# Kernel optimization log

Hardware: AMD Instinct MI355X
Metric: run time of the kernel (lower is better)

The kernel has to match this reference:

```python
import jax, jax.numpy as jnp
import numpy as np

NEG = -1e9  # large negative used as log(0) to keep grads finite
EPS = 1e-38


def _pcfg_inside(theta_log, Phi):
    # theta_log: [N,N,N] (A -> B C), Phi: [B,N,T] log terminal probs
    B, N, T = Phi.shape
    tm = jnp.max(theta_log)
    et = jnp.exp(theta_log - tm)  # [A,Bn,Cn], all > 0
    beta = jnp.full((B, N, T, T), NEG, dtype=Phi.dtype)
    idx = jnp.arange(T)
    beta = beta.at[:, :, idx, idx].set(Phi)  # length-1 spans
    for l in range(2, T + 1):
        P = T - l + 1
        ii = jnp.arange(P)
        ss = jnp.arange(l - 1)
        lcol = ii[:, None] + ss[None, :]          # left child end  [P,S]
        left = beta[:, :, ii[:, None], lcol]      # [B,N,P,S]
        right = beta[:, :, lcol + 1, (ii + l - 1)[:, None]]  # [B,N,P,S]
        ml = jnp.max(left, axis=1)                # [B,P,S]
        mr = jnp.max(right, axis=1)
        el = jnp.exp(left - ml[:, None])
        er = jnp.exp(right - mr[:, None])
        inner = jnp.einsum('xyz,byps,bzps->bxps', et, el, er)
        sc = jnp.log(jnp.maximum(inner, EPS)) + tm + ml[:, None] + mr[:, None]
        score = jax.scipy.special.logsumexp(sc, axis=-1)  # over split points -> [B,N,P]
        beta = beta.at[:, :, ii, ii + l - 1].set(score)
    logZ = beta[:, 0, 0, T - 1]  # start symbol id 0, full span
    return beta, logZ


def _pcfg_outside(theta_log, beta):
    B, N, T, _ = beta.shape
    tm = jnp.max(theta_log)
    et = jnp.exp(theta_log - tm)
    alpha = jnp.full((B, N, T, T), NEG, dtype=beta.dtype)
    alpha = alpha.at[:, 0, 0, T - 1].set(0.0)
    for l in range(T, 1, -1):  # parent spans, longest first
        P = T - l + 1
        ii = jnp.arange(P)
        jj = ii + l - 1
        ss = jnp.arange(l - 1)
        lcol = ii[:, None] + ss[None, :]          # left child end  [P,S]
        rrow = lcol + 1                            # right child start
        a = alpha[:, :, ii, jj]                    # [B,N,P]
        lb = beta[:, :, ii[:, None], lcol]         # [B,N,P,S]
        rb = beta[:, :, rrow, jj[:, None]]         # [B,N,P,S]
        ma = jnp.max(a, axis=1)                    # [B,P]
        ea = jnp.exp(a - ma[:, None])
        mrb = jnp.max(rb, axis=1)
        erb = jnp.exp(rb - mrb[:, None])
        mlb = jnp.max(lb, axis=1)
        elb = jnp.exp(lb - mlb[:, None])
        cL = jnp.log(jnp.maximum(jnp.einsum('xyz,bxp,bzps->byps', et, ea, erb), EPS)) \
             + tm + ma[:, None, :, None] + mrb[:, None]
        cR = jnp.log(jnp.maximum(jnp.einsum('xyz,bxp,byps->bzps', et, ea, elb), EPS)) \
             + tm + ma[:, None, :, None] + mlb[:, None]
        alpha = alpha.at[:, :, ii[:, None], lcol].set(
            jnp.logaddexp(alpha[:, :, ii[:, None], lcol], cL))
        alpha = alpha.at[:, :, rrow, jj[:, None]].set(
            jnp.logaddexp(alpha[:, :, rrow, jj[:, None]], cR))
    return alpha


def setup_inputs() -> dict:
    key = jax.random.key(0)
    ks = jax.random.split(key, 6)
    B, T, k, N, V = 16, 32, 512, 24, 32000
    g_seq = jax.random.normal(ks[0], (B, T, k), dtype=jnp.float32)
    Theta = jax.random.normal(ks[1], (N, N, N), dtype=jnp.float32) * 0.01
    nt2vocab = (jax.random.uniform(ks[2], (N, V), dtype=jnp.float32) < 0.05).astype(jnp.float32)
    ln_gamma = jnp.ones((k,), jnp.float32)
    ln_beta = jnp.zeros((k,), jnp.float32)
    W1 = jax.random.normal(ks[3], (k, 128), dtype=jnp.float32) * 0.02
    b1 = jnp.zeros((128,), jnp.float32)
    W2 = jax.random.normal(ks[4], (128, N), dtype=jnp.float32) * 0.02
    b2 = jnp.zeros((N,), jnp.float32)
    return {"g_seq": g_seq, "Theta": Theta, "nt2vocab": nt2vocab,
            "ln_gamma": ln_gamma, "ln_beta": ln_beta,
            "W1": W1, "b1": b1, "W2": W2, "b2": b2}


def reference(g_seq, Theta, nt2vocab, ln_gamma, ln_beta, W1, b1, W2, b2):
    # term head: LayerNorm -> Linear(k,128) -> GELU(exact) -> Linear(128,N)
    mu = jnp.mean(g_seq, axis=-1, keepdims=True)
    var = jnp.var(g_seq, axis=-1, keepdims=True)  # biased, as torch LayerNorm
    g = (g_seq - mu) / jnp.sqrt(var + 1e-5) * ln_gamma + ln_beta
    h = jax.nn.gelu(g @ W1 + b1, approximate=False)
    out = h @ W2 + b2                                # [B,T,N]
    Phi = jax.nn.log_softmax(out.transpose(0, 2, 1), axis=1)   # [B,N,T]
    theta_log = jax.nn.log_softmax(Theta, axis=-1)   # softmax over flattened (B,C) last dim == axis -1 of [N,N,N] after view(-1,N)
    N = Theta.shape[0]
    theta_log = jax.nn.log_softmax(Theta.reshape(-1, N), axis=-1).reshape(N, N, N)
    beta, logZ = _pcfg_inside(theta_log, Phi)
    alpha = _pcfg_outside(theta_log, beta)
    T = Phi.shape[2]
    idx = jnp.arange(T)
    p_nt = jnp.exp(alpha[:, :, idx, idx] + beta[:, :, idx, idx] - logZ[:, None, None])  # [B,N,T]
    mask_logits = jnp.log(1e-6 + jnp.einsum('bnt,nv->btv', p_nt, nt2vocab))
    L_pcfg = (-logZ).mean()
    return mask_logits, L_pcfg
```

## Files before the change

### kernel.cpp

```cpp
#include <hip/hip_runtime.h>
#include <math.h>

#define NEGV -1000000000.0f
#define EPSV 1e-38f

typedef _Float16 h16;
typedef _Float16 h2 __attribute__((ext_vector_type(2)));
typedef _Float16 h4 __attribute__((ext_vector_type(4)));

constexpr int BSTRIDE = 528 * 32;
constexpr int ASTRIDE = 528 * 24;

constexpr int O_WK   = 28032;
constexpr int O_EA   = 28032;
constexpr int O_EBF  = 31008;
constexpr int O_EB16 = 33984;
constexpr int O_RR   = 35472;
constexpr int O_RED2 = 36656;
constexpr int O_MRL  = 37424;
constexpr int O_MSM  = 37552;
constexpr int O_SCAL = 37680;
constexpr int SMEM_SZ = 37744;

__device__ __forceinline__ int tri(int i, int j) { return ((j * (j + 1)) >> 1) + i; }
__device__ __forceinline__ float la2(float a, float c) {
  float mx = fmaxf(a, c), mn = fminf(a, c);
  return mx + log1pf(__expf(mn - mx));
}
__device__ __forceinline__ void gstore(float* p, float v) {
  __hip_atomic_store(p, v, __ATOMIC_RELAXED, __HIP_MEMORY_SCOPE_AGENT);
}
__device__ __forceinline__ float gload(const float* p) {
  return __hip_atomic_load(p, __ATOMIC_RELAXED, __HIP_MEMORY_SCOPE_AGENT);
}
__device__ __forceinline__ void storeu(unsigned* p, unsigned v) {
  __hip_atomic_store(p, v, __ATOMIC_RELAXED, __HIP_MEMORY_SCOPE_AGENT);
}
__device__ __forceinline__ unsigned loadu(const unsigned* p) {
  return __hip_atomic_load(p, __ATOMIC_RELAXED, __HIP_MEMORY_SCOPE_AGENT);
}
__device__ __forceinline__ float d2(h16 ax, h16 ay, h16 bx, h16 by, float c) {
#if __has_builtin(__builtin_amdgcn_fdot2)
  h2 a; a.x = ax; a.y = ay;
  h2 b; b.x = bx; b.y = by;
  return __builtin_amdgcn_fdot2(a, b, c, false);
#else
  return c + (float)ax * (float)bx + (float)ay * (float)by;
#endif
}

__global__ void __launch_bounds__(256, 2) mega_kernel(
    const float* __restrict__ g_seq, const float* __restrict__ Theta,
    const float* __restrict__ vocab, const float* __restrict__ lng,
    const float* __restrict__ lnb, const float* __restrict__ W1,
    const float* __restrict__ bb1, const float* __restrict__ W2,
    const float* __restrict__ bb2, float* __restrict__ out,
    float* __restrict__ et_g, float* __restrict__ beta_g,
    float* __restrict__ aL_g, float* __restrict__ aR_g,
    unsigned* __restrict__ cnt, float* __restrict__ logZg) {
  __shared__ __align__(16) unsigned char smem[SMEM_SZ];
  h16* et16h = (h16*)smem;
  float* wk = (float*)(smem + O_WK);
  const int tid = threadIdx.x;
  const int blk = blockIdx.x;
  const int b = blk & 15, local = blk >> 4;
  unsigned* gcnt  = cnt;
  unsigned* done  = cnt + 8;
  unsigned* ibc   = cnt + 16 + b * 16;
  unsigned* slotI = cnt + 512 + b * 64;
  unsigned* slotO = slotI + 32;
  float* bbase = beta_g + b * BSTRIDE;
  float* aLb = aL_g + b * ASTRIDE;
  float* aRb = aR_g + b * ASTRIDE;

  {
    float* g = wk;
    float2* red = (float2*)(wk + 512);
    float* hb = wk + 1024;
    float* ob = wk + 1152;
    float* sc = wk + 1184;
    float2 raw = ((const float2*)(g_seq + (size_t)blk * 512))[tid];
    red[tid] = make_float2(raw.x + raw.y, raw.x * raw.x + raw.y * raw.y);
    __syncthreads();
    if (tid < 128) { float2 o = red[tid + 128], m = red[tid]; red[tid] = make_float2(m.x + o.x, m.y + o.y); }
    __syncthreads();
    if (tid < 64) {
      float2 v = red[tid], o = red[tid + 64];
      v.x += o.x; v.y += o.y;
      for (int off = 32; off; off >>= 1) { v.x += __shfl_xor(v.x, off); v.y += __shfl_xor(v.y, off); }
      if (tid == 0) {
        float mu = v.x / 512.0f;
        float var = v.y / 512.0f - mu * mu;
        sc[0] = mu; sc[1] = rsqrtf(var + 1e-5f);
      }
    }
    __syncthreads();
    float mu = sc[0], rstd = sc[1];
    g[2 * tid]     = (raw.x - mu) * rstd * lng[2 * tid]     + lnb[2 * tid];
    g[2 * tid + 1] = (raw.y - mu) * rstd * lng[2 * tid + 1] + lnb[2 * tid + 1];
    __syncthreads();
    {
      int j = tid & 127, hh = tid >> 7, c0 = hh * 256;
      float a0 = 0, a1 = 0, a2 = 0, a3 = 0;
      for (int c = 0; c < 256; c += 4) {
        a0 = fmaf(g[c0 + c],     W1[(c0 + c) * 128 + j],     a0);
        a1 = fmaf(g[c0 + c + 1], W1[(c0 + c + 1) * 128 + j], a1);
        a2 = fmaf(g[c0 + c + 2], W1[(c0 + c + 2) * 128 + j], a2);
        a3 = fmaf(g[c0 + c + 3], W1[(c0 + c + 3) * 128 + j], a3);
      }
      ((float*)red)[tid] = (a0 + a1) + (a2 + a3);
    }
    __syncthreads();
    if (tid < 128) {
      float a = ((float*)red)[tid] + ((float*)red)[tid + 128] + bb1[tid];
      hb[tid] = 0.5f * a * (1.0f + erff(a * 0.70710678118654752f));
    }
    __syncthreads();
    if (tid < 192) {
      int n = tid >> 3, q = tid & 7;
      float a = 0;
      for (int k = 0; k < 16; k++) a = fmaf(hb[q * 16 + k], W2[(q * 16 + k) * 24 + n], a);
      ((float*)red)[tid] = a;
    }
    __syncthreads();
    if (tid < 24) {
      float a = bb2[tid];
      for (int q = 0; q < 8; q++) a += ((float*)red)[tid * 8 + q];
      ob[tid] = a;
    }
    __syncthreads();
    if (tid == 0) {
      float m = ob[0];
      for (int n = 1; n < 24; n++) m = fmaxf(m, ob[n]);
      float s = 0;
      for (int n = 0; n < 24; n++) s += __expf(ob[n] - m);
      sc[2] = m + __logf(s);
    }
    __syncthreads();
    if (tid < 24) {
      int fb = blk >> 5, ft = blk & 31;
      gstore(beta_g + (size_t)fb * BSTRIDE + tri(ft, ft) * 32 + tid, ob[tid] - sc[2]);
    }
  }
  if (tid < 64) {
    int z = tid & 31;
    bool up = tid >= 32;
    int row = up ? (512 + blk) : blk;
    bool valid = (!up) || (blk < 64);
    float v = (z < 24 && valid) ? Theta[row * 24 + z] : NEGV;
    float m = v;
    for (int off = 16; off; off >>= 1) m = fmaxf(m, __shfl_xor(m, off));
    float e = (z < 24 && valid) ? __expf(v - m) : 0.f;
    float s = e;
    for (int off = 16; off; off >>= 1) s += __shfl_xor(s, off);
    float lse = m + __logf(s);
    if (z < 24 && valid) gstore(et_g + row * 24 + z, __expf(v - lse));
  }
  for (int idx = blk * 256 + tid; idx < 2 * 16 * ASTRIDE; idx += 131072) {
    float v = NEGV;
    if (idx < 16 * ASTRIDE && (idx % ASTRIDE) == 11904) v = 0.f;
    gstore(aL_g + idx, v);
  }
  __builtin_amdgcn_s_waitcnt(0);
  __syncthreads();
  if (tid == 0) {
    __hip_atomic_fetch_add(ibc, 1u, __ATOMIC_RELAXED, __HIP_MEMORY_SCOPE_AGENT);
    if (local == 0) {
      while (loadu(ibc) < 32u) __builtin_amdgcn_s_sleep(2);
      __hip_atomic_fetch_add(gcnt, 1u, __ATOMIC_RELAXED, __HIP_MEMORY_SCOPE_AGENT);
    }
    while (loadu(gcnt) < 16u) __builtin_amdgcn_s_sleep(2);
  }
  __syncthreads();

  for (int i4 = tid; i4 < 3456; i4 += 256) {
    int f = i4 * 4;
    int x = f / 576, r = f - x * 576;
    float4 v = ((const float4*)et_g)[i4];
    h4 t; t.x = (h16)v.x; t.y = (h16)v.y; t.z = (h16)v.z; t.w = (h16)v.w;
    *(h4*)(et16h + x * 584 + r) = t;
  }
  __syncthreads();

  {
    float* eA   = (float*)(smem + O_EA);
    float* eBf  = (float*)(smem + O_EBF);
    h16*  eb16  = (h16*)(smem + O_EB16);
    h16*  rrh   = (h16*)(smem + O_RR);
    float* red2 = (float*)(smem + O_RED2);
    float* mrl  = (float*)(smem + O_MRL);
    float* msm  = (float*)(smem + O_MSM);
    float* scal = (float*)(smem + O_SCAL);
    const int lastLI = 32 - local;
    for (int l = 2; l <= lastLI; l++) {
      int S = l - 1;
      if (l >= 3 && tid == 0) {
        unsigned need = (unsigned)(l - 1);
        while (loadu(slotI + local + 1) < need) __builtin_amdgcn_s_sleep(1);
      }
      __syncthreads();
      {
        int i = local, j = i + S, SN = S * 24;
        for (int idx4 = tid; idx4 < 6 * S; idx4 += 256) {
          int s = idx4 / 6, q = idx4 - 6 * s;
          ((float4*)eA)[idx4]  = ((const float4*)(bbase + (size_t)tri(i, i + s) * 32))[q];
          ((float4*)eBf)[idx4] = ((const float4*)(bbase + (size_t)tri(i + s + 1, j) * 32))[q];
        }
        __syncthreads();
        if (tid < 8 * S) {
          int s = tid >> 3, q = tid & 7, y0 = q * 3;
          float pa = fmaxf(fmaxf(eA[s * 24 + y0], eA[s * 24 + y0 + 1]), eA[s * 24 + y0 + 2]);
          float pb = fmaxf(fmaxf(eBf[s * 24 + y0], eBf[s * 24 + y0 + 1]), eBf[s * 24 + y0 + 2]);
          for (int off = 4; off; off >>= 1) {
            pa = fmaxf(pa, __shfl_xor(pa, off));
            pb = fmaxf(pb, __shfl_xor(pb, off));
          }
          if (q == 0) { mrl[s] = pb; msm[s] = pa + pb; }
        }
        __syncthreads();
        if (tid < 32) {
          float v = (tid < S) ? msm[tid] : NEGV;
          for (int off = 16; off; off >>= 1) v = fmaxf(v, __shfl_xor(v, off));
          if (tid == 0) scal[0] = v;
        }
        __syncthreads();
        float M = scal[0];
        for (int idx = tid; idx < SN; idx += 256) {
          int s = idx / 24;
          float m_ = mrl[s];
          eA[idx] = __expf(eA[idx] + m_ - M);
          eb16[idx] = (h16)__expf(eBf[idx] - m_);
        }
        __syncthreads();
        if (tid < 144) {
          int y = tid / 6, zq = tid % 6;
          float4 acc = make_float4(0, 0, 0, 0);
          for (int s = 0; s < S; s++) {
            float a = eA[s * 24 + y];
            h4 b4 = ((const h4*)(eb16 + s * 24))[zq];
            acc.x = fmaf(a, (float)b4.x, acc.x); acc.y = fmaf(a, (float)b4.y, acc.y);
            acc.z = fmaf(a, (float)b4.z, acc.z); acc.w = fmaf(a, (float)b4.w, acc.w);
          }
          h4 t; t.x = (h16)acc.x; t.y = (h16)acc.y; t.z = (h16)acc.z; t.w = (h16)acc.w;
          ((h4*)(rrh + y * 24))[zq] = t;
        }
        __syncthreads();
        if (tid < 192) {
          int x = tid >> 3, c = tid & 7;
          const h4* e4 = (const h4*)(et16h + x * 584 + c * 72);
          const h4* r4 = (const h4*)(rrh + c * 72);
          float a0 = 0, a1 = 0;
#pragma unroll
          for (int q = 0; q < 18; q += 2) {
            h4 ev = e4[q], rv = r4[q];
            a0 = d2(ev.x, ev.y, rv.x, rv.y, a0);
            a0 = d2(ev.z, ev.w, rv.z, rv.w, a0);
            h4 e2 = e4[q + 1], r2v = r4[q + 1];
            a1 = d2(e2.x, e2.y, r2v.x, r2v.y, a1);
            a1 = d2(e2.z, e2.w, r2v.z, r2v.w, a1);
          }
          red2[tid] = a0 + a1;
        }
        __syncthreads();
        if (tid < 24) {
          float a = 0;
          for (int q = 0; q < 8; q++) a += red2[tid * 8 + q];
          gstore(bbase + (size_t)tri(i, j) * 32 + tid, M + __logf(fmaxf(a, EPSV)));
        }
      }
      __builtin_amdgcn_s_waitcnt(0);
      __syncthreads();
      if (tid == 0) storeu(slotI + local, (unsigned)l);
    }
  }
  if (local == 0 && tid == 0) {
    gstore(logZg + b, gload(bbase + 496 * 32));
    __hip_atomic_fetch_add(done, 1u, __ATOMIC_RELAXED, __HIP_MEMORY_SCOPE_AGENT);
  }

  {
    float* ebL  = (float*)(smem + O_EA);
    float* ebRf = (float*)(smem + O_EBF);
    h16*  eb16  = (h16*)(smem + O_EB16);
    h16*  rrh   = (h16*)(smem + O_RR);
    float* ea24 = (float*)(smem + O_RED2);
    float* mLs  = (float*)(smem + O_MRL);
    float* mRs  = (float*)(smem + O_MSM);
    float* scal = (float*)(smem + O_SCAL);
    const int lastLO = 32 - local;
    for (int l = lastLO; l >= 2; l--) {
      int S = l - 1;
      if (local > 0 && tid == 0) {
        unsigned need = (unsigned)(32 - l);
        while (loadu(slotO + local - 1) < need) __builtin_amdgcn_s_sleep(1);
      }
      __syncthreads();
      {
        int i = local, j = i + S, SN = S * 24;
        if (tid < 32) {
          float av = NEGV;
          if (tid < 24) av = la2(gload(aLb + tri(i, j) * 24 + tid), gload(aRb + tri(i, j) * 24 + tid));
          float m = av;
          for (int off = 16; off; off >>= 1) m = fmaxf(m, __shfl_xor(m, off));
          if (tid < 24) ea24[tid] = __expf(av - m);
          if (tid == 0) scal[0] = m;
        }
        __syncthreads();
        float ma = scal[0];
        if (tid < 144) {
          int y = tid / 6, zq = tid % 6;
          float4 acc = make_float4(0, 0, 0, 0);
#pragma unroll 4
          for (int x = 0; x < 24; x++) {
            float a = ea24[x];
            h4 ev = ((const h4*)(et16h + x * 584 + y * 24))[zq];
            acc.x = fmaf(a, (float)ev.x, acc.x); acc.y = fmaf(a, (float)ev.y, acc.y);
            acc.z = fmaf(a, (float)ev.z, acc.z); acc.w = fmaf(a, (float)ev.w, acc.w);
          }
          h4 t; t.x = (h16)acc.x; t.y = (h16)acc.y; t.z = (h16)acc.z; t.w = (h16)acc.w;
          ((h4*)(rrh + y * 24))[zq] = t;
        }
        for (int idx4 = tid; idx4 < 6 * S; idx4 += 256) {
          int s = idx4 / 6, q = idx4 - 6 * s;
          ((float4*)ebL)[idx4]  = ((const float4*)(bbase + (size_t)tri(i, i + s) * 32))[q];
          ((float4*)ebRf)[idx4] = ((const float4*)(bbase + (size_t)tri(i + s + 1, j) * 32))[q];
        }
        __syncthreads();
        if (tid < 8 * S) {
          int s = tid >> 3, q = tid & 7, y0 = q * 3;
          float pl = fmaxf(fmaxf(ebL[s * 24 + y0], ebL[s * 24 + y0 + 1]), ebL[s * 24 + y0 + 2]);
          float pr = fmaxf(fmaxf(ebRf[s * 24 + y0], ebRf[s * 24 + y0 + 1]), ebRf[s * 24 + y0 + 2]);
          for (int off = 4; off; off >>= 1) {
            pl = fmaxf(pl, __shfl_xor(pl, off));
            pr = fmaxf(pr, __shfl_xor(pr, off));
          }
          if (q == 0) { mLs[s] = pl; mRs[s] = pr; }
        }
        __syncthreads();
        for (int idx = tid; idx < SN; idx += 256) {
          int s = idx / 24;
          ebL[idx] = __expf(ebL[idx] - mLs[s]);
          eb16[idx] = (h16)__expf(ebRf[idx] - mRs[s]);
        }
        __syncthreads();
        for (int u = tid; u < 2 * SN; u += 256) {
          if (u < SN) {
            int s = u / 24, y = u - s * 24;
            const h4* w4 = (const h4*)(rrh + y * 24);
            const h4* r4 = (const h4*)(eb16 + s * 24);
            float acc = 0;
#pragma unroll
            for (int q = 0; q < 6; q++) {
              h4 a = w4[q], c4 = r4[q];
              acc = d2(a.x, a.y, c4.x, c4.y, acc);
              acc = d2(a.z, a.w, c4.z, c4.w, acc);
            }
            float val = __logf(fmaxf(acc, EPSV)) + ma + mRs[s];
            float* t = aLb + tri(i, i + s) * 24 + y;
            gstore(t, la2(gload(t), val));
          } else {
            int u2 = u - SN;
            int s = u2 / 24, z = u2 - s * 24;
            float acc = 0;
            for (int y = 0; y < 24; y++) acc = fmaf((float)rrh[y * 24 + z], ebL[s * 24 + y], acc);
            float val = __logf(fmaxf(acc, EPSV)) + ma + mLs[s];
            float* t = aRb + tri(i + s + 1, j) * 24 + z;
            gstore(t, la2(gload(t), val));
          }
        }
      }
      __builtin_amdgcn_s_waitcnt(0);
      __syncthreads();
      if (tid == 0) storeu(slotO + local, (unsigned)(33 - l));
    }
  }
  if (tid < 64) {
    for (;;) {
      unsigned v = 31;
      if (tid < 31) v = loadu(slotO + tid);
      if (__ballot(v >= 31u) == ~0ull) break;
      __builtin_amdgcn_s_sleep(1);
    }
  }
  __syncthreads();

  {
    float* p = (float*)smem;
    float logZv = gload(bbase + 496 * 32);
    for (int c = tid; c < 768; c += 256) {
      int n = c >> 5, t = c & 31;
      int dA = tri(t, t) * 24 + n;
      float al = gload(aLb + dA), ar = gload(aRb + dA);
      p[c] = __expf(la2(al, ar) + bbase[(size_t)tri(t, t) * 32 + n] - logZv);
    }
    __syncthreads();
    int vbase = local * 1000;
    for (int pass = 0; pass < 2; pass++) {
      int o0 = tid + pass * 512, o1 = o0 + 256;
      bool v0ok = o0 < 1000, v1ok = o1 < 1000;
      int v0 = vbase + o0, v1 = vbase + o1;
      float vr0[24], vr1[24];
#pragma unroll
      for (int n = 0; n < 24; n++) {
        vr0[n] = v0ok ? vocab[n * 32000 + v0] : 0.f;
        vr1[n] = v1ok ? vocab[n * 32000 + v1] : 0.f;
      }
      float* ob0 = out + (size_t)b * 32 * 32000 + v0;
      float* ob1 = out + (size_t)b * 32 * 32000 + v1;
      for (int t4 = 0; t4 < 32; t4 += 4) {
        float a00 = 1e-6f, a01 = 1e-6f, a02 = 1e-6f, a03 = 1e-6f;
        float a10 = 1e-6f, a11 = 1e-6f, a12 = 1e-6f, a13 = 1e-6f;
#pragma unroll 6
        for (int n = 0; n < 24; n++) {
          float4 pv = *(const float4*)(p + n * 32 + t4);
          a00 = fmaf(pv.x, vr0[n], a00); a01 = fmaf(pv.y, vr0[n], a01);
          a02 = fmaf(pv.z, vr0[n], a02); a03 = fmaf(pv.w, vr0[n], a03);
          a10 = fmaf(pv.x, vr1[n], a10); a11 = fmaf(pv.y, vr1[n], a11);
          a12 = fmaf(pv.z, vr1[n], a12); a13 = fmaf(pv.w, vr1[n], a13);
        }
        if (v0ok) {
          ob0[(size_t)(t4 + 0) * 32000] = __logf(a00);
          ob0[(size_t)(t4 + 1) * 32000] = __logf(a01);
          ob0[(size_t)(t4 + 2) * 32000] = __logf(a02);
          ob0[(size_t)(t4 + 3) * 32000] = __logf(a03);
        }
        if (v1ok) {
          ob1[(size_t)(t4 + 0) * 32000] = __logf(a10);
          ob1[(size_t)(t4 + 1) * 32000] = __logf(a11);
          ob1[(size_t)(t4 + 2) * 32000] = __logf(a12);
          ob1[(size_t)(t4 + 3) * 32000] = __logf(a13);
        }
      }
    }
    if (blk == 0 && tid == 0) {
      while (loadu(done) < 16u) __builtin_amdgcn_s_sleep(2);
      float s = 0;
      for (int q = 0; q < 16; q++) s += gload(logZg + q);
      out[16384000] = -s / 16.0f;
    }
  }
}

extern "C" void kernel_launch(void* const* d_in, const int* in_sizes, int n_in,
                              void* d_out, int out_size, void* d_ws, size_t ws_size,
                              hipStream_t stream) {
  (void)in_sizes; (void)n_in; (void)out_size; (void)ws_size;
  const float* g_seq = (const float*)d_in[0];
  const float* Theta = (const float*)d_in[1];
  const float* vocab = (const float*)d_in[2];
  const float* lng   = (const float*)d_in[3];
  const float* lnb   = (const float*)d_in[4];
  const float* W1    = (const float*)d_in[5];
  const float* bb1   = (const float*)d_in[6];
  const float* W2    = (const float*)d_in[7];
  const float* bb2   = (const float*)d_in[8];
  float* out = (float*)d_out;

  float* ws = (float*)d_ws;
  unsigned* cnt = (unsigned*)d_ws;
  float* logZg  = ws + 2048;
  float* et_g   = ws + 4096;
  float* beta_g = ws + 18432;
  float* aL_g   = beta_g + 16 * BSTRIDE;
  float* aR_g   = aL_g + 16 * ASTRIDE;

  hipMemsetAsync(d_ws, 0, 8192, stream);

  void* args[] = {(void*)&g_seq, (void*)&Theta, (void*)&vocab, (void*)&lng,
                  (void*)&lnb, (void*)&W1, (void*)&bb1, (void*)&W2, (void*)&bb2,
                  (void*)&out, (void*)&et_g, (void*)&beta_g, (void*)&aL_g,
                  (void*)&aR_g, (void*)&cnt, (void*)&logZg};
  hipLaunchCooperativeKernel((const void*)mega_kernel, dim3(512), dim3(256),
                             args, 0, stream);
}
```

Measured before the change: 479.6 us.

## Replace inside-pass progress counters with per-cell sentinel dataflow sync and overlap outside stages

The inside pass drops the per-span-length slot counters. Beta cells are pre-filled with a NaN sentinel, and consumers spin on the actual cell data, so each block waits only for the cells it needs rather than a whole neighbour step. The outside pass now runs the alpha reduction in parallel with the child loads and the rule-contraction product. It also releases its progress slot after the right-child updates, before the left-child updates, so the next block starts earlier. Max reductions and the final theta dot product are restructured with fewer threads and barriers, and the vocab loads for the output stage are prefetched before the final wait. The risks are heavier polling traffic on global beta and the correctness assumptions behind the early slot release.

```diff
diff --git a/kernel.cpp b/kernel.cpp
--- a/kernel.cpp
+++ b/kernel.cpp
@@ -3,6 +3,7 @@
 
 #define NEGV -1000000000.0f
 #define EPSV 1e-38f
+#define SENTU 0x7FC00001u
 
 typedef _Float16 h16;
 typedef _Float16 h2 __attribute__((ext_vector_type(2)));
@@ -16,7 +17,7 @@
 constexpr int O_EBF  = 31008;
 constexpr int O_EB16 = 33984;
 constexpr int O_RR   = 35472;
-constexpr int O_RED2 = 36656;
+constexpr int O_EA24 = 36656;
 constexpr int O_MRL  = 37424;
 constexpr int O_MSM  = 37552;
 constexpr int O_SCAL = 37680;
@@ -48,6 +49,16 @@
   return c + (float)ax * (float)bx + (float)ay * (float)by;
 #endif
 }
+__device__ __forceinline__ float wmax64(float v) {
+#pragma unroll
+  for (int off = 32; off; off >>= 1) v = fmaxf(v, __shfl_xor(v, off));
+  return v;
+}
+
+#define MAX12(A, B, C)                                                        \
+  fmaxf(fmaxf(fmaxf(fmaxf(A.x, A.y), fmaxf(A.z, A.w)),                        \
+              fmaxf(fmaxf(B.x, B.y), fmaxf(B.z, B.w))),                       \
+        fmaxf(fmaxf(C.x, C.y), fmaxf(C.z, C.w)))
 
 __global__ void __launch_bounds__(256, 2) mega_kernel(
     const float* __restrict__ g_seq, const float* __restrict__ Theta,
@@ -67,8 +78,7 @@
   unsigned* gcnt  = cnt;
   unsigned* done  = cnt + 8;
   unsigned* ibc   = cnt + 16 + b * 16;
-  unsigned* slotI = cnt + 512 + b * 64;
-  unsigned* slotO = slotI + 32;
+  unsigned* slotO = cnt + 512 + b * 64 + 32;
   float* bbase = beta_g + b * BSTRIDE;
   float* aLb = aL_g + b * ASTRIDE;
   float* aRb = aR_g + b * ASTRIDE;
@@ -161,6 +171,19 @@
     if (idx < 16 * ASTRIDE && (idx % ASTRIDE) == 11904) v = 0.f;
     gstore(aL_g + idx, v);
   }
+  for (int idx = blk * 256 + tid; idx < 16 * BSTRIDE; idx += 131072) {
+    int w = idx % BSTRIDE;
+    int cell = w >> 5, wic = w & 31;
+    if (wic >= 24) continue;
+    int t0 = (int)((sqrtf(8.f * (float)cell + 9.f) - 3.f) * 0.5f + 0.5f);
+    bool isDiag = false;
+#pragma unroll
+    for (int dt = -1; dt <= 1; ++dt) {
+      int t = t0 + dt;
+      if (t >= 0 && ((t * (t + 3)) >> 1) == cell) isDiag = true;
+    }
+    if (!isDiag) gstore(beta_g + idx, __uint_as_float(SENTU));
+  }
   __builtin_amdgcn_s_waitcnt(0);
   __syncthreads();
   if (tid == 0) {
@@ -187,94 +210,87 @@
     float* eBf  = (float*)(smem + O_EBF);
     h16*  eb16  = (h16*)(smem + O_EB16);
     h16*  rrh   = (h16*)(smem + O_RR);
-    float* red2 = (float*)(smem + O_RED2);
     float* mrl  = (float*)(smem + O_MRL);
-    float* msm  = (float*)(smem + O_MSM);
     float* scal = (float*)(smem + O_SCAL);
     const int lastLI = 32 - local;
     for (int l = 2; l <= lastLI; l++) {
       int S = l - 1;
-      if (l >= 3 && tid == 0) {
-        unsigned need = (unsigned)(l - 1);
-        while (loadu(slotI + local + 1) < need) __builtin_amdgcn_s_sleep(1);
-      }
-      __syncthreads();
-      {
-        int i = local, j = i + S, SN = S * 24;
-        for (int idx4 = tid; idx4 < 6 * S; idx4 += 256) {
-          int s = idx4 / 6, q = idx4 - 6 * s;
-          ((float4*)eA)[idx4]  = ((const float4*)(bbase + (size_t)tri(i, i + s) * 32))[q];
-          ((float4*)eBf)[idx4] = ((const float4*)(bbase + (size_t)tri(i + s + 1, j) * 32))[q];
-        }
-        __syncthreads();
-        if (tid < 8 * S) {
-          int s = tid >> 3, q = tid & 7, y0 = q * 3;
-          float pa = fmaxf(fmaxf(eA[s * 24 + y0], eA[s * 24 + y0 + 1]), eA[s * 24 + y0 + 2]);
-          float pb = fmaxf(fmaxf(eBf[s * 24 + y0], eBf[s * 24 + y0 + 1]), eBf[s * 24 + y0 + 2]);
-          for (int off = 4; off; off >>= 1) {
-            pa = fmaxf(pa, __shfl_xor(pa, off));
-            pb = fmaxf(pb, __shfl_xor(pb, off));
-          }
-          if (q == 0) { mrl[s] = pb; msm[s] = pa + pb; }
-        }
-        __syncthreads();
-        if (tid < 32) {
-          float v = (tid < S) ? msm[tid] : NEGV;
-          for (int off = 16; off; off >>= 1) v = fmaxf(v, __shfl_xor(v, off));
-          if (tid == 0) scal[0] = v;
-        }
-        __syncthreads();
-        float M = scal[0];
-        for (int idx = tid; idx < SN; idx += 256) {
-          int s = idx / 24;
-          float m_ = mrl[s];
-          eA[idx] = __expf(eA[idx] + m_ - M);
-          eb16[idx] = (h16)__expf(eBf[idx] - m_);
-        }
-        __syncthreads();
-        if (tid < 144) {
-          int y = tid / 6, zq = tid % 6;
-          float4 acc = make_float4(0, 0, 0, 0);
-          for (int s = 0; s < S; s++) {
-            float a = eA[s * 24 + y];
-            h4 b4 = ((const h4*)(eb16 + s * 24))[zq];
-            acc.x = fmaf(a, (float)b4.x, acc.x); acc.y = fmaf(a, (float)b4.y, acc.y);
-            acc.z = fmaf(a, (float)b4.z, acc.z); acc.w = fmaf(a, (float)b4.w, acc.w);
-          }
-          h4 t; t.x = (h16)acc.x; t.y = (h16)acc.y; t.z = (h16)acc.z; t.w = (h16)acc.w;
-          ((h4*)(rrh + y * 24))[zq] = t;
-        }
-        __syncthreads();
-        if (tid < 192) {
-          int x = tid >> 3, c = tid & 7;
-          const h4* e4 = (const h4*)(et16h + x * 584 + c * 72);
-          const h4* r4 = (const h4*)(rrh + c * 72);
-          float a0 = 0, a1 = 0;
-#pragma unroll
-          for (int q = 0; q < 18; q += 2) {
-            h4 ev = e4[q], rv = r4[q];
-            a0 = d2(ev.x, ev.y, rv.x, rv.y, a0);
-            a0 = d2(ev.z, ev.w, rv.z, rv.w, a0);
-            h4 e2 = e4[q + 1], r2v = r4[q + 1];
-            a1 = d2(e2.x, e2.y, r2v.x, r2v.y, a1);
-            a1 = d2(e2.z, e2.w, r2v.z, r2v.w, a1);
-          }
-          red2[tid] = a0 + a1;
-        }
-        __syncthreads();
-        if (tid < 24) {
-          float a = 0;
-          for (int q = 0; q < 8; q++) a += red2[tid * 8 + q];
-          gstore(bbase + (size_t)tri(i, j) * 32 + tid, M + __logf(fmaxf(a, EPSV)));
-        }
+      int i = local, j = i + S, SN = S * 24;
+      for (int idx4 = tid; idx4 < 6 * S; idx4 += 256) {
+        int s = idx4 / 6, q = idx4 - 6 * s;
+        ((float4*)eA)[idx4] = ((const float4*)(bbase + (size_t)tri(i, i + s) * 32))[q];
+        const float* cp = bbase + (size_t)tri(i + s + 1, j) * 32 + q * 4;
+        float w0 = gload(cp), w1 = gload(cp + 1), w2 = gload(cp + 2), w3 = gload(cp + 3);
+        while ((__float_as_uint(w0) == SENTU) | (__float_as_uint(w1) == SENTU) |
+               (__float_as_uint(w2) == SENTU) | (__float_as_uint(w3) == SENTU)) {
+          __builtin_amdgcn_s_sleep(1);
+          w0 = gload(cp); w1 = gload(cp + 1); w2 = gload(cp + 2); w3 = gload(cp + 3);
+        }
+        float4 t4; t4.x = w0; t4.y = w1; t4.z = w2; t4.w = w3;
+        ((float4*)eBf)[idx4] = t4;
+      }
+      __syncthreads();
+      if (tid < 64) {
+        int s = tid >> 1, h12 = tid & 1;
+        float pa = NEGV, pb = NEGV;
+        if (s < S) {
+          const float4* ra = (const float4*)(eA + s * 24 + h12 * 12);
+          float4 A = ra[0], B = ra[1], C = ra[2];
+          pa = MAX12(A, B, C);
+          const float4* rb = (const float4*)(eBf + s * 24 + h12 * 12);
+          float4 D = rb[0], E = rb[1], F = rb[2];
+          pb = MAX12(D, E, F);
+        }
+        pa = fmaxf(pa, __shfl_xor(pa, 1));
+        pb = fmaxf(pb, __shfl_xor(pb, 1));
+        if (s < S && h12 == 0) mrl[s] = pb;
+        float M0 = wmax64((s < S) ? pa + pb : NEGV);
+        if (tid == 0) scal[0] = M0;
+      }
+      __syncthreads();
+      float M = scal[0];
+      for (int idx = tid; idx < SN; idx += 256) {
+        int s = idx / 24;
+        float m_ = mrl[s];
+        eA[idx] = __expf(eA[idx] + m_ - M);
+        eb16[idx] = (h16)__expf(eBf[idx] - m_);
+      }
+      __syncthreads();
+      if (tid < 144) {
+        int y = tid / 6, zq = tid % 6;
+        float4 acc = make_float4(0, 0, 0, 0);
+        for (int s = 0; s < S; s++) {
+          float a = eA[s * 24 + y];
+          h4 b4 = ((const h4*)(eb16 + s * 24))[zq];
+          acc.x = fmaf(a, (float)b4.x, acc.x); acc.y = fmaf(a, (float)b4.y, acc.y);
+          acc.z = fmaf(a, (float)b4.z, acc.z); acc.w = fmaf(a, (float)b4.w, acc.w);
+        }
+        h4 t; t.x = (h16)acc.x; t.y = (h16)acc.y; t.z = (h16)acc.z; t.w = (h16)acc.w;
+        ((h4*)(rrh + y * 24))[zq] = t;
+      }
+      __syncthreads();
+      if (tid < 48) {
+        int x = tid >> 1, hh = tid & 1;
+        const h4* ep = (const h4*)(et16h + x * 584 + hh * 288);
+        const h4* rp = (const h4*)(rrh + hh * 288);
+        float a2 = 0.f;
+#pragma unroll 8
+        for (int q = 0; q < 72; ++q) {
+          h4 ev = ep[q], rv = rp[q];
+          a2 = d2(ev.x, ev.y, rv.x, rv.y, a2);
+          a2 = d2(ev.z, ev.w, rv.z, rv.w, a2);
+        }
+        a2 += __shfl_xor(a2, 1);
+        if (hh == 0)
+          gstore(bbase + (size_t)tri(i, j) * 32 + x, M + __logf(fmaxf(a2, EPSV)));
       }
       __builtin_amdgcn_s_waitcnt(0);
       __syncthreads();
-      if (tid == 0) storeu(slotI + local, (unsigned)l);
     }
   }
   if (local == 0 && tid == 0) {
     gstore(logZg + b, gload(bbase + 496 * 32));
+    __builtin_amdgcn_s_waitcnt(0);
     __hip_atomic_fetch_add(done, 1u, __ATOMIC_RELAXED, __HIP_MEMORY_SCOPE_AGENT);
   }
 
@@ -283,108 +299,123 @@
     float* ebRf = (float*)(smem + O_EBF);
     h16*  eb16  = (h16*)(smem + O_EB16);
     h16*  rrh   = (h16*)(smem + O_RR);
-    float* ea24 = (float*)(smem + O_RED2);
+    float* ea24 = (float*)(smem + O_EA24);
     float* mLs  = (float*)(smem + O_MRL);
     float* mRs  = (float*)(smem + O_MSM);
     float* scal = (float*)(smem + O_SCAL);
     const int lastLO = 32 - local;
     for (int l = lastLO; l >= 2; l--) {
       int S = l - 1;
+      int i = local, j = i + S, SN = S * 24;
       if (local > 0 && tid == 0) {
         unsigned need = (unsigned)(32 - l);
         while (loadu(slotO + local - 1) < need) __builtin_amdgcn_s_sleep(1);
       }
-      __syncthreads();
-      {
-        int i = local, j = i + S, SN = S * 24;
-        if (tid < 32) {
-          float av = NEGV;
-          if (tid < 24) av = la2(gload(aLb + tri(i, j) * 24 + tid), gload(aRb + tri(i, j) * 24 + tid));
-          float m = av;
-          for (int off = 16; off; off >>= 1) m = fmaxf(m, __shfl_xor(m, off));
-          if (tid < 24) ea24[tid] = __expf(av - m);
-          if (tid == 0) scal[0] = m;
-        }
-        __syncthreads();
-        float ma = scal[0];
-        if (tid < 144) {
-          int y = tid / 6, zq = tid % 6;
-          float4 acc = make_float4(0, 0, 0, 0);
-#pragma unroll 4
-          for (int x = 0; x < 24; x++) {
-            float a = ea24[x];
-            h4 ev = ((const h4*)(et16h + x * 584 + y * 24))[zq];
-            acc.x = fmaf(a, (float)ev.x, acc.x); acc.y = fmaf(a, (float)ev.y, acc.y);
-            acc.z = fmaf(a, (float)ev.z, acc.z); acc.w = fmaf(a, (float)ev.w, acc.w);
-          }
-          h4 t; t.x = (h16)acc.x; t.y = (h16)acc.y; t.z = (h16)acc.z; t.w = (h16)acc.w;
-          ((h4*)(rrh + y * 24))[zq] = t;
-        }
-        for (int idx4 = tid; idx4 < 6 * S; idx4 += 256) {
+      __builtin_amdgcn_s_waitcnt(0);
+      __syncthreads();
+      if (tid < 64) {
+        float av = NEGV;
+        if (tid < 24)
+          av = la2(gload(aLb + tri(i, j) * 24 + tid), gload(aRb + tri(i, j) * 24 + tid));
+        float mav = wmax64(av);
+        if (tid < 24) ea24[tid] = __expf(av - mav);
+        if (tid == 0) scal[0] = mav;
+      } else {
+        for (int idx4 = tid - 64; idx4 < 6 * S; idx4 += 192) {
           int s = idx4 / 6, q = idx4 - 6 * s;
           ((float4*)ebL)[idx4]  = ((const float4*)(bbase + (size_t)tri(i, i + s) * 32))[q];
           ((float4*)ebRf)[idx4] = ((const float4*)(bbase + (size_t)tri(i + s + 1, j) * 32))[q];
         }
-        __syncthreads();
-        if (tid < 8 * S) {
-          int s = tid >> 3, q = tid & 7, y0 = q * 3;
-          float pl = fmaxf(fmaxf(ebL[s * 24 + y0], ebL[s * 24 + y0 + 1]), ebL[s * 24 + y0 + 2]);
-          float pr = fmaxf(fmaxf(ebRf[s * 24 + y0], ebRf[s * 24 + y0 + 1]), ebRf[s * 24 + y0 + 2]);
-          for (int off = 4; off; off >>= 1) {
-            pl = fmaxf(pl, __shfl_xor(pl, off));
-            pr = fmaxf(pr, __shfl_xor(pr, off));
-          }
-          if (q == 0) { mLs[s] = pl; mRs[s] = pr; }
-        }
-        __syncthreads();
-        for (int idx = tid; idx < SN; idx += 256) {
-          int s = idx / 24;
-          ebL[idx] = __expf(ebL[idx] - mLs[s]);
-          eb16[idx] = (h16)__expf(ebRf[idx] - mRs[s]);
-        }
-        __syncthreads();
-        for (int u = tid; u < 2 * SN; u += 256) {
-          if (u < SN) {
-            int s = u / 24, y = u - s * 24;
-            const h4* w4 = (const h4*)(rrh + y * 24);
-            const h4* r4 = (const h4*)(eb16 + s * 24);
-            float acc = 0;
+      }
+      __syncthreads();
+      float ma = scal[0];
+      if (tid < 64) {
+        int s = tid >> 1, h12 = tid & 1;
+        float pl = NEGV, pr = NEGV;
+        if (s < S) {
+          const float4* ra = (const float4*)(ebL + s * 24 + h12 * 12);
+          float4 A = ra[0], B = ra[1], C = ra[2];
+          pl = MAX12(A, B, C);
+          const float4* rb = (const float4*)(ebRf + s * 24 + h12 * 12);
+          float4 D = rb[0], E = rb[1], F = rb[2];
+          pr = MAX12(D, E, F);
+        }
+        pl = fmaxf(pl, __shfl_xor(pl, 1));
+        pr = fmaxf(pr, __shfl_xor(pr, 1));
+        if (s < S && h12 == 0) { mLs[s] = pl; mRs[s] = pr; }
+      } else if (tid < 208) {
+        int t = tid - 64, y = t / 6, zq = t % 6;
+        float4 acc = make_float4(0, 0, 0, 0);
+#pragma unroll 4
+        for (int x = 0; x < 24; x++) {
+          float a = ea24[x];
+          h4 ev = ((const h4*)(et16h + x * 584 + y * 24))[zq];
+          acc.x = fmaf(a, (float)ev.x, acc.x); acc.y = fmaf(a, (float)ev.y, acc.y);
+          acc.z = fmaf(a, (float)ev.z, acc.z); acc.w = fmaf(a, (float)ev.w, acc.w);
+        }
+        h4 t4; t4.x = (h16)acc.x; t4.y = (h16)acc.y; t4.z = (h16)acc.z; t4.w = (h16)acc.w;
+        ((h4*)(rrh + y * 24))[zq] = t4;
+      }
+      __syncthreads();
+      for (int idx = tid; idx < SN; idx += 256) {
+        int s = idx / 24;
+        ebL[idx] = __expf(ebL[idx] - mLs[s]);
+        eb16[idx] = (h16)__expf(ebRf[idx] - mRs[s]);
+      }
+      __syncthreads();
+      for (int u = tid; u < SN; u += 256) {
+        int s = u / 24, z = u - s * 24;
+        float acc = 0;
+        for (int y = 0; y < 24; y++) acc = fmaf((float)rrh[y * 24 + z], ebL[s * 24 + y], acc);
+        float val = __logf(fmaxf(acc, EPSV)) + ma + mLs[s];
+        float* t = aRb + tri(i + s + 1, j) * 24 + z;
+        gstore(t, la2(gload(t), val));
+      }
+      __builtin_amdgcn_s_waitcnt(0);
+      __syncthreads();
+      if (tid == 0) storeu(slotO + local, (unsigned)(33 - l));
+      for (int u = tid; u < SN; u += 256) {
+        int s = u / 24, y = u - s * 24;
+        const h4* w4 = (const h4*)(rrh + y * 24);
+        const h4* r4 = (const h4*)(eb16 + s * 24);
+        float acc = 0;
 #pragma unroll
-            for (int q = 0; q < 6; q++) {
-              h4 a = w4[q], c4 = r4[q];
-              acc = d2(a.x, a.y, c4.x, c4.y, acc);
-              acc = d2(a.z, a.w, c4.z, c4.w, acc);
-            }
-            float val = __logf(fmaxf(acc, EPSV)) + ma + mRs[s];
-            float* t = aLb + tri(i, i + s) * 24 + y;
-            gstore(t, la2(gload(t), val));
-          } else {
-            int u2 = u - SN;
-            int s = u2 / 24, z = u2 - s * 24;
-            float acc = 0;
-            for (int y = 0; y < 24; y++) acc = fmaf((float)rrh[y * 24 + z], ebL[s * 24 + y], acc);
-            float val = __logf(fmaxf(acc, EPSV)) + ma + mLs[s];
-            float* t = aRb + tri(i + s + 1, j) * 24 + z;
-            gstore(t, la2(gload(t), val));
-          }
-        }
-      }
-      __builtin_amdgcn_s_waitcnt(0);
-      __syncthreads();
-      if (tid == 0) storeu(slotO + local, (unsigned)(33 - l));
-    }
-  }
-  if (tid < 64) {
-    for (;;) {
-      unsigned v = 31;
-      if (tid < 31) v = loadu(slotO + tid);
-      if (__ballot(v >= 31u) == ~0ull) break;
-      __builtin_amdgcn_s_sleep(1);
-    }
-  }
-  __syncthreads();
+        for (int q = 0; q < 6; q++) {
+          h4 a = w4[q], c4 = r4[q];
+          acc = d2(a.x, a.y, c4.x, c4.y, acc);
+          acc = d2(a.z, a.w, c4.z, c4.w, acc);
+        }
+        float val = __logf(fmaxf(acc, EPSV)) + ma + mRs[s];
+        float* t = aLb + tri(i, i + s) * 24 + y;
+        gstore(t, la2(gload(t), val));
+      }
+    }
+    __builtin_amdgcn_s_waitcnt(0);
+    __syncthreads();
+    if (tid == 0) storeu(slotO + local, 32u);
+  }
 
   {
+    int vbase = local * 1000;
+    float pv0[24], pv1[24];
+    {
+      int o0 = tid, o1 = tid + 256;
+      bool k0 = o0 < 1000, k1 = o1 < 1000;
+#pragma unroll
+      for (int n = 0; n < 24; n++) {
+        pv0[n] = k0 ? vocab[n * 32000 + vbase + o0] : 0.f;
+        pv1[n] = k1 ? vocab[n * 32000 + vbase + o1] : 0.f;
+      }
+    }
+    if (tid < 64) {
+      for (;;) {
+        unsigned v = 32;
+        if (tid < 31) v = loadu(slotO + tid);
+        if (__ballot(v >= 32u) == ~0ull) break;
+        __builtin_amdgcn_s_sleep(1);
+      }
+    }
+    __syncthreads();
     float* p = (float*)smem;
     float logZv = gload(bbase + 496 * 32);
     for (int c = tid; c < 768; c += 256) {
@@ -394,16 +425,16 @@
       p[c] = __expf(la2(al, ar) + bbase[(size_t)tri(t, t) * 32 + n] - logZv);
     }
     __syncthreads();
-    int vbase = local * 1000;
     for (int pass = 0; pass < 2; pass++) {
       int o0 = tid + pass * 512, o1 = o0 + 256;
       bool v0ok = o0 < 1000, v1ok = o1 < 1000;
       int v0 = vbase + o0, v1 = vbase + o1;
-      float vr0[24], vr1[24];
+      if (pass == 1) {
 #pragma unroll
-      for (int n = 0; n < 24; n++) {
-        vr0[n] = v0ok ? vocab[n * 32000 + v0] : 0.f;
-        vr1[n] = v1ok ? vocab[n * 32000 + v1] : 0.f;
+        for (int n = 0; n < 24; n++) {
+          pv0[n] = v0ok ? vocab[n * 32000 + v0] : 0.f;
+          pv1[n] = v1ok ? vocab[n * 32000 + v1] : 0.f;
+        }
       }
       float* ob0 = out + (size_t)b * 32 * 32000 + v0;
       float* ob1 = out + (size_t)b * 32 * 32000 + v1;
@@ -413,10 +444,10 @@
 #pragma unroll 6
         for (int n = 0; n < 24; n++) {
           float4 pv = *(const float4*)(p + n * 32 + t4);
-          a00 = fmaf(pv.x, vr0[n], a00); a01 = fmaf(pv.y, vr0[n], a01);
-          a02 = fmaf(pv.z, vr0[n], a02); a03 = fmaf(pv.w, vr0[n], a03);
-          a10 = fmaf(pv.x, vr1[n], a10); a11 = fmaf(pv.y, vr1[n], a11);
-          a12 = fmaf(pv.z, vr1[n], a12); a13 = fmaf(pv.w, vr1[n], a13);
+          a00 = fmaf(pv.x, pv0[n], a00); a01 = fmaf(pv.y, pv0[n], a01);
+          a02 = fmaf(pv.z, pv0[n], a02); a03 = fmaf(pv.w, pv0[n], a03);
+          a10 = fmaf(pv.x, pv1[n], a10); a11 = fmaf(pv.y, pv1[n], a11);
+          a12 = fmaf(pv.z, pv1[n], a12); a13 = fmaf(pv.w, pv1[n], a13);
         }
         if (v0ok) {
           ob0[(size_t)(t4 + 0) * 32000] = __logf(a00);
```

Result: faster. 439.0 us (-8.5%).
